# Kernel optimization log

Measured on AMD Instinct MI355X. Metric: run time of the kernel, lower is better.

The kernel has to match this reference:

```python
import jax, jax.numpy as jnp
import numpy as np


def _apply_gates(iou, c_in):
    # iou: [..., 3H]; c_in: [..., H]  (TreeLSTMCell.apply_node_func)
    i, o, u = jnp.split(iou, 3, axis=-1)
    c = jax.nn.sigmoid(i) * jnp.tanh(u) + c_in
    h = jax.nn.sigmoid(o) * jnp.tanh(c)
    return h, c


def setup_inputs() -> dict:
    key = jax.random.key(0)
    ks = jax.random.split(key, 10)
    V, X, H, C = 32000, 300, 256, 5
    B, L = 64, 2048  # 64 perfect binary trees, 2048 leaves each
    s = lambda n: 1.0 / np.sqrt(n)
    return {
        "wordid": jax.random.randint(ks[0], (B, L), 0, V),
        "emb": jax.random.normal(ks[1], (V, X), jnp.float32) * 0.1,
        "W_iou": jax.random.normal(ks[2], (X, 3 * H), jnp.float32) * s(X),
        "b_Wiou": jnp.zeros((3 * H,), jnp.float32),
        "U_iou": jax.random.normal(ks[3], (2 * H, 3 * H), jnp.float32) * s(2 * H),
        "b_Uiou": jnp.zeros((3 * H,), jnp.float32),
        "U_f": jax.random.normal(ks[4], (2 * H, 2 * H), jnp.float32) * s(2 * H),
        "b_Uf": jnp.zeros((2 * H,), jnp.float32),
        "W_out": jax.random.normal(ks[5], (H, C), jnp.float32) * s(H),
        "b_out": jnp.zeros((C,), jnp.float32),
    }


def reference(wordid, emb, W_iou, b_Wiou, U_iou, b_Uiou, U_f, b_Uf, W_out, b_out):
    B, L = wordid.shape
    H = W_out.shape[0]
    # --- leaves: x = W_iou(embed(word)); initial c = 0 ---
    x = emb[wordid]                               # [B, L, X] gather
    iou = x @ W_iou + b_Wiou                      # [B, L, 3H]
    h, c = _apply_gates(iou, jnp.zeros((B, L, H), iou.dtype))
    h_levels = [h.reshape(B * L, H)]
    n = L
    # --- propagate up the tree (topological levels) ---
    while n > 1:
        n //= 2
        h_cat = h.reshape(B, n, 2 * H)            # concat(left,right) per parent
        c_pair = c.reshape(B, n, 2, H)
        f = jax.nn.sigmoid(h_cat @ U_f + b_Uf).reshape(B, n, 2, H)
        c_f = jnp.sum(f * c_pair, axis=2)         # [B, n, H]
        iou = h_cat @ U_iou + b_Uiou              # [B, n, 3H]
        h, c = _apply_gates(iou, c_f)
        h_levels.append(h.reshape(B * n, H))
    h_all = jnp.concatenate(h_levels, axis=0)     # [N_total, H] (level-major)
    # dropout is identity in eval mode
    return h_all @ W_out + b_out                  # [N_total, num_classes]
```

## Files before the change

kernel.cpp:

```cpp
#include <hip/hip_runtime.h>
#include <hip/hip_bf16.h>

typedef __attribute__((ext_vector_type(8))) short bfrag8;
typedef __attribute__((ext_vector_type(4))) float f32x4;

#define DIV_UP(a,b) (((a)+(b)-1)/(b))

__device__ __forceinline__ float sigm(float x){ return 1.0f/(1.0f + __expf(-x)); }
__device__ __forceinline__ float fast_tanh(float x){
  float ax = fabsf(x);
  float t = __expf(-2.0f*ax);
  float r = (1.0f - t)/(1.0f + t);
  return copysignf(r, x);
}
__device__ __forceinline__ float bf2f(short s){
  unsigned int u = ((unsigned int)(unsigned short)s) << 16;
  return __uint_as_float(u);
}
__device__ __forceinline__ unsigned short f2bf_bits(float x){
  __hip_bfloat16 b = __float2bfloat16(x);
  return *reinterpret_cast<unsigned short*>(&b);
}

#define GLOAD_LDS16(g, l) \
  __builtin_amdgcn_global_load_lds((const __attribute__((address_space(1))) void*)(g), \
                                   (__attribute__((address_space(3))) void*)(l), 16, 0, 0)

__global__ void conv_emb4(const float* __restrict__ e, __hip_bfloat16* __restrict__ o){
  int idx = blockIdx.x*256 + threadIdx.x;
  if (idx >= 32000*80) return;
  int v = idx / 80, c = idx - v*80;
  ushort4 r;
  if (c < 75) {
    float4 f = *(const float4*)(e + (size_t)v*300 + c*4);
    r.x = f2bf_bits(f.x); r.y = f2bf_bits(f.y); r.z = f2bf_bits(f.z); r.w = f2bf_bits(f.w);
  } else { r.x = r.y = r.z = r.w = 0; }
  *(ushort4*)((unsigned short*)o + (size_t)v*320 + c*4) = r;
}
__global__ void conv_wiou_i(const float* __restrict__ Wf, __hip_bfloat16* __restrict__ o){
  int idx = blockIdx.x*256 + threadIdx.x;
  if (idx >= 768*320) return;
  int n = idx / 320, k = idx - n*320;
  int eg = n / 48, rem = n - eg*48, gate = rem >> 4, es = rem & 15;
  int e = eg*16 + es;
  o[idx] = __float2bfloat16(k < 300 ? Wf[(size_t)k*768 + gate*256 + e] : 0.0f);
}
__global__ void conv_ucat_i(const float* __restrict__ Ui, const float* __restrict__ Uf,
                            __hip_bfloat16* __restrict__ o){
  int idx = blockIdx.x*256 + threadIdx.x;
  if (idx >= 1280*512) return;
  int n = idx >> 9, k = idx & 511;
  int eg = n / 80, rem = n - eg*80, gate = rem >> 4, es = rem & 15;
  int e = eg*16 + es;
  float v = (gate < 3) ? Ui[(size_t)k*768 + gate*256 + e]
                       : Uf[(size_t)k*512 + (gate-3)*256 + e];
  o[idx] = __float2bfloat16(v);
}

template<int NG, bool G2>
__global__ __launch_bounds__(256, 3) void gemm_fused(
    const char* __restrict__ Ab,
    const int*  __restrict__ wid,
    const char* __restrict__ Btb,
    int M, int K, int Kb,
    const float* __restrict__ b_iou,
    const float* __restrict__ b_f,
    const float* __restrict__ cprev,
    __hip_bfloat16* __restrict__ Hout, float* __restrict__ Cout)
{
  constexpr int GW  = NG*16;
  constexpr int BN  = 2*GW;
  constexpr int BCH = BN*4;
  constexpr int BUF = 8192 + BN*64;
  __shared__ __align__(16) char lds[2*BUF];

  const int lx = blockIdx.y & 7;
  const int ly = ((blockIdx.y >> 3) << 3) | (blockIdx.x & 7);
  const int row0 = ly*128;
  if (row0 >= M) return;

  const int t = threadIdx.x, lane = t & 63, w = t >> 6;
  const int wr = w >> 1, wc = w & 1;
  const int frow = lane & 15, g = lane >> 4;
  const size_t colbase = (size_t)lx * BN;
  const size_t Kbyt = (size_t)K*2;

  const char* abase0[2]; const char* abase1[2];
  #pragma unroll
  for (int i = 0; i < 2; ++i) {
    int c = t + i*256;
    int rp = c >> 3, lc = (c & 7) ^ (rp & 7);
    int r = rp*2 + (lc >> 2), q = lc & 3;
    int row = row0 + r; row = row < M ? row : M-1;
    if constexpr (G2) {
      abase0[i] = Ab + (size_t)wid[2*row]  *512 + q*16;
      abase1[i] = Ab + (size_t)wid[2*row+1]*512 + q*16 - 512;
    } else {
      abase0[i] = Ab + (size_t)row*Kb + q*16;
      abase1[i] = abase0[i];
    }
  }
  const char* bbase[3];
  const int nb = (t < 128) ? ((NG==5) ? 3 : 2) : ((NG==5) ? 2 : 1);
  #pragma unroll
  for (int i = 0; i < 3; ++i) {
    int cb = t + i*256;
    if (cb < BCH) {
      int rp = cb >> 3, lc = (cb & 7) ^ (rp & 7);
      int r = rp*2 + (lc >> 2), q = lc & 3;
      bbase[i] = Btb + (colbase + r)*Kbyt + q*16;
    } else bbase[i] = Btb;
  }

  auto STAGE = [&](int b, int ks){
    const int kb0 = ks*64;
    char* la = lds + b*BUF;
    char* lb = la + 8192;
    #pragma unroll
    for (int i = 0; i < 2; ++i) {
      const char* s = (G2 && kb0 >= 512) ? abase1[i] + kb0 : abase0[i] + kb0;
      GLOAD_LDS16(s, la + (t + i*256)*16);
    }
    #pragma unroll
    for (int i = 0; i < 3; ++i)
      if (i < nb) GLOAD_LDS16(bbase[i] + kb0, lb + (t + i*256)*16);
  };

  const int fr2 = frow >> 1;
  const int pc  = (((frow & 1)*4 + g) ^ (fr2 & 7));
  const int aoff = wr*4096 + fr2*128 + pc*16;
  const int boff = wc*(GW*64) + fr2*128 + pc*16;

  f32x4 acc[4][NG] = {};
  const int nsteps = K >> 5;

  STAGE(0, 0);
  for (int ks = 0; ks < nsteps; ++ks) {
    const int b = ks & 1;
    if (ks + 1 < nsteps) {
      STAGE(b ^ 1, ks + 1);
      if constexpr (NG == 5) {
        if (w < 2) asm volatile("s_waitcnt vmcnt(5)" ::: "memory");
        else       asm volatile("s_waitcnt vmcnt(4)" ::: "memory");
      } else {
        if (w < 2) asm volatile("s_waitcnt vmcnt(4)" ::: "memory");
        else       asm volatile("s_waitcnt vmcnt(3)" ::: "memory");
      }
    } else {
      asm volatile("s_waitcnt vmcnt(0)" ::: "memory");
    }
    __builtin_amdgcn_s_barrier();
    asm volatile("" ::: "memory");

    const char* la = lds + b*BUF;
    const char* lb = la + 8192;
    bfrag8 af[4], bfv[NG];
    #pragma unroll
    for (int mi = 0; mi < 4; ++mi) af[mi] = *(const bfrag8*)(la + aoff + mi*1024);
    #pragma unroll
    for (int gi = 0; gi < NG; ++gi) bfv[gi] = *(const bfrag8*)(lb + boff + gi*1024);
    #pragma unroll
    for (int mi = 0; mi < 4; ++mi)
      #pragma unroll
      for (int gi = 0; gi < NG; ++gi)
        acc[mi][gi] = __builtin_amdgcn_mfma_f32_16x16x32_bf16(af[mi], bfv[gi], acc[mi][gi], 0, 0, 0);

    asm volatile("" ::: "memory");
    __builtin_amdgcn_s_barrier();
  }

  const int e = lx*32 + wc*16 + frow;
  const float bi = b_iou[e], bo = b_iou[256+e], bu = b_iou[512+e];
  float bf0 = 0.f, bf1 = 0.f;
  if constexpr (NG == 5) { bf0 = b_f[e]; bf1 = b_f[256+e]; }
  #pragma unroll
  for (int mi = 0; mi < 4; ++mi) {
    const int mb = row0 + wr*64 + mi*16 + g*4;
    #pragma unroll
    for (int r = 0; r < 4; ++r) {
      const int m = mb + r;
      if (m < M) {
        float cv = sigm(acc[mi][0][r] + bi) * fast_tanh(acc[mi][2][r] + bu);
        if constexpr (NG == 5) {
          const size_t c0i = G2 ? (size_t)wid[2*m]   : (size_t)(2*m);
          const size_t c1i = G2 ? (size_t)wid[2*m+1] : (size_t)(2*m+1);
          cv += sigm(acc[mi][3][r] + bf0) * cprev[c0i*256 + e]
              + sigm(acc[mi][4][r] + bf1) * cprev[c1i*256 + e];
        }
        Cout[(size_t)m*256 + e] = cv;
        Hout[(size_t)m*256 + e] = __float2bfloat16(sigm(acc[mi][1][r] + bo) * fast_tanh(cv));
      }
    }
  }
}

__global__ void outproj_v(const __hip_bfloat16* __restrict__ h, int M,
                          const float* __restrict__ Wout, const float* __restrict__ bout,
                          float* __restrict__ out){
  const int t = threadIdx.x;
  const int half = t >> 5, l32 = t & 31;
  const int e0 = l32 * 8;
  float wv[8][5];
  #pragma unroll
  for (int j = 0; j < 8; ++j)
    #pragma unroll
    for (int cl = 0; cl < 5; ++cl) wv[j][cl] = Wout[(e0+j)*5 + cl];
  const float b0 = bout[0], b1 = bout[1], b2 = bout[2], b3 = bout[3], b4 = bout[4];
  for (int row = blockIdx.x*8 + half; row < M; row += gridDim.x*8) {
    bfrag8 hv = *(const bfrag8*)((const short*)h + (size_t)row*256 + e0);
    float a0=0,a1=0,a2=0,a3=0,a4=0;
    #pragma unroll
    for (int j = 0; j < 8; ++j) {
      float x = bf2f(hv[j]);
      a0 += x*wv[j][0]; a1 += x*wv[j][1]; a2 += x*wv[j][2]; a3 += x*wv[j][3]; a4 += x*wv[j][4];
    }
    #pragma unroll
    for (int off = 16; off; off >>= 1) {
      a0 += __shfl_down(a0, off); a1 += __shfl_down(a1, off);
      a2 += __shfl_down(a2, off); a3 += __shfl_down(a3, off); a4 += __shfl_down(a4, off);
    }
    if (l32 == 0) {
      float* op = out + (size_t)row*5;
      op[0]=a0+b0; op[1]=a1+b1; op[2]=a2+b2; op[3]=a3+b3; op[4]=a4+b4;
    }
  }
}

__global__ void leaf_scatter(const int* __restrict__ wid, const float* __restrict__ outvoc,
                             float* __restrict__ out){
  int p = blockIdx.x*256 + threadIdx.x;
  if (p >= 131072) return;
  const float* s = outvoc + (size_t)wid[p]*5;
  float* d = out + (size_t)p*5;
  #pragma unroll
  for (int j = 0; j < 5; ++j) d[j] = s[j];
}

extern "C" void kernel_launch(void* const* d_in, const int* in_sizes, int n_in,
                              void* d_out, int out_size, void* d_ws, size_t ws_size,
                              hipStream_t stream) {
  const int* wordid   = (const int*)d_in[0];
  const float* emb    = (const float*)d_in[1];
  const float* W_iou  = (const float*)d_in[2];
  const float* b_Wiou = (const float*)d_in[3];
  const float* U_iou  = (const float*)d_in[4];
  const float* b_Uiou = (const float*)d_in[5];
  const float* U_f    = (const float*)d_in[6];
  const float* b_Uf   = (const float*)d_in[7];
  const float* W_out  = (const float*)d_in[8];
  const float* b_out  = (const float*)d_in[9];
  float* out = (float*)d_out;

  char* p = (char*)d_ws;
  auto take = [&](size_t bytes){ char* r = p; p += (bytes + 255) & ~(size_t)255; return r; };
  __hip_bfloat16* wiouT  = (__hip_bfloat16*)take((size_t)768*320*2);
  __hip_bfloat16* ucatT  = (__hip_bfloat16*)take((size_t)1280*512*2);
  __hip_bfloat16* h_voc  = (__hip_bfloat16*)take((size_t)32000*256*2);
  float*          c_voc  = (float*)take((size_t)32000*256*4);
  float*          outvoc = (float*)take((size_t)32000*5*4);
  __hip_bfloat16* hAll   = (__hip_bfloat16*)take((size_t)131008*256*2);
  float*          cA     = (float*)take((size_t)65536*256*4);
  float*          cB     = (float*)take((size_t)32768*256*4);
  __hip_bfloat16* embbf  = (__hip_bfloat16*)cA;

  auto ceil8 = [](int y){ return (y + 7) & ~7; };

  conv_emb4  <<<DIV_UP(32000*80, 256),256,0,stream>>>(emb, embbf);
  conv_wiou_i<<<DIV_UP(768*320,  256),256,0,stream>>>(W_iou, wiouT);
  conv_ucat_i<<<DIV_UP(1280*512, 256),256,0,stream>>>(U_iou, U_f, ucatT);

  gemm_fused<3,false><<<dim3(8,ceil8(250)),256,0,stream>>>(
      (const char*)embbf, nullptr, (const char*)wiouT, 32000, 320, 640,
      b_Wiou, nullptr, nullptr, h_voc, c_voc);
  outproj_v<<<1024,256,0,stream>>>(h_voc, 32000, W_out, b_out, outvoc);
  leaf_scatter<<<DIV_UP(131072,256),256,0,stream>>>(wordid, outvoc, out);

  gemm_fused<5,true><<<dim3(8,512),256,0,stream>>>(
      (const char*)h_voc, wordid, (const char*)ucatT, 65536, 512, 0,
      b_Uiou, b_Uf, c_voc, hAll, cA);

  const __hip_bfloat16* hp = hAll; const float* cp = cA;
  size_t hoff = 65536;
  int Mlvl = 65536;
  for (int lvl = 2; lvl <= 11; ++lvl) {
    Mlvl >>= 1;
    float* cn = (lvl & 1) ? cA : cB;
    gemm_fused<5,false><<<dim3(8,ceil8(DIV_UP(Mlvl,128))),256,0,stream>>>(
        (const char*)hp, nullptr, (const char*)ucatT, Mlvl, 512, 1024,
        b_Uiou, b_Uf, cp, hAll + hoff*256, cn);
    hp = hAll + hoff*256; cp = cn; hoff += Mlvl;
  }

  outproj_v<<<2048,256,0,stream>>>(hAll, 131008, W_out, b_out, out + (size_t)131072*5);
}
```

Baseline: 480.4 us.

## Load A fragments directly to registers and quad-buffer B tiles in LDS

After: 634.1 us. +32.0%, slower.

```diff
diff --git a/kernel.cpp b/kernel.cpp
--- a/kernel.cpp
+++ b/kernel.cpp
@@ -68,11 +68,11 @@
     const float* __restrict__ cprev,
     __hip_bfloat16* __restrict__ Hout, float* __restrict__ Cout)
 {
-  constexpr int GW  = NG*16;
-  constexpr int BN  = 2*GW;
-  constexpr int BCH = BN*4;
-  constexpr int BUF = 8192 + BN*64;
-  __shared__ __align__(16) char lds[2*BUF];
+  constexpr int GW   = NG*16;
+  constexpr int BN   = 2*GW;
+  constexpr int BCH  = BN*4;
+  constexpr int BUFB = BN*64;
+  __shared__ __align__(16) char lds[4*BUFB];
 
   const int lx = blockIdx.y & 7;
   const int ly = ((blockIdx.y >> 3) << 3) | (blockIdx.x & 7);
@@ -85,21 +85,6 @@
   const size_t colbase = (size_t)lx * BN;
   const size_t Kbyt = (size_t)K*2;
 
-  const char* abase0[2]; const char* abase1[2];
-  #pragma unroll
-  for (int i = 0; i < 2; ++i) {
-    int c = t + i*256;
-    int rp = c >> 3, lc = (c & 7) ^ (rp & 7);
-    int r = rp*2 + (lc >> 2), q = lc & 3;
-    int row = row0 + r; row = row < M ? row : M-1;
-    if constexpr (G2) {
-      abase0[i] = Ab + (size_t)wid[2*row]  *512 + q*16;
-      abase1[i] = Ab + (size_t)wid[2*row+1]*512 + q*16 - 512;
-    } else {
-      abase0[i] = Ab + (size_t)row*Kb + q*16;
-      abase1[i] = abase0[i];
-    }
-  }
   const char* bbase[3];
   const int nb = (t < 128) ? ((NG==5) ? 3 : 2) : ((NG==5) ? 2 : 1);
   #pragma unroll
@@ -112,15 +97,31 @@
     } else bbase[i] = Btb;
   }
 
-  auto STAGE = [&](int b, int ks){
-    const int kb0 = ks*64;
-    char* la = lds + b*BUF;
-    char* lb = la + 8192;
-    #pragma unroll
-    for (int i = 0; i < 2; ++i) {
-      const char* s = (G2 && kb0 >= 512) ? abase1[i] + kb0 : abase0[i] + kb0;
-      GLOAD_LDS16(s, la + (t + i*256)*16);
-    }
+  int aoff0[4], aoff1[4];
+  #pragma unroll
+  for (int mi = 0; mi < 4; ++mi) {
+    int row = row0 + wr*64 + mi*16 + frow;
+    row = row < M ? row : M-1;
+    if constexpr (G2) {
+      aoff0[mi] = wid[2*row]*512 + g*16;
+      aoff1[mi] = wid[2*row+1]*512 + g*16 - 512;
+    } else {
+      aoff0[mi] = row*Kb + g*16;
+      aoff1[mi] = aoff0[mi];
+    }
+  }
+
+  bfrag8 af[4];
+  auto ALD = [&](int kb0){
+    #pragma unroll
+    for (int mi = 0; mi < 4; ++mi) {
+      int off = (G2 && kb0 >= 512) ? aoff1[mi] : aoff0[mi];
+      af[mi] = *(const bfrag8*)(Ab + (size_t)(kb0 + off));
+    }
+  };
+  auto BST = [&](int buf, int ks2){
+    const int kb0 = ks2*64;
+    char* lb = lds + buf*BUFB;
     #pragma unroll
     for (int i = 0; i < 3; ++i)
       if (i < nb) GLOAD_LDS16(bbase[i] + kb0, lb + (t + i*256)*16);
@@ -128,35 +129,34 @@
 
   const int fr2 = frow >> 1;
   const int pc  = (((frow & 1)*4 + g) ^ (fr2 & 7));
-  const int aoff = wr*4096 + fr2*128 + pc*16;
   const int boff = wc*(GW*64) + fr2*128 + pc*16;
 
   f32x4 acc[4][NG] = {};
   const int nsteps = K >> 5;
 
-  STAGE(0, 0);
+  BST(0, 0);
+  ALD(0);
+  BST(1, 1);
+
   for (int ks = 0; ks < nsteps; ++ks) {
-    const int b = ks & 1;
     if (ks + 1 < nsteps) {
-      STAGE(b ^ 1, ks + 1);
       if constexpr (NG == 5) {
-        if (w < 2) asm volatile("s_waitcnt vmcnt(5)" ::: "memory");
-        else       asm volatile("s_waitcnt vmcnt(4)" ::: "memory");
+        if (w < 2) asm volatile("s_waitcnt vmcnt(7)" ::: "memory");
+        else       asm volatile("s_waitcnt vmcnt(6)" ::: "memory");
       } else {
-        if (w < 2) asm volatile("s_waitcnt vmcnt(4)" ::: "memory");
-        else       asm volatile("s_waitcnt vmcnt(3)" ::: "memory");
+        if (w < 2) asm volatile("s_waitcnt vmcnt(6)" ::: "memory");
+        else       asm volatile("s_waitcnt vmcnt(5)" ::: "memory");
       }
     } else {
-      asm volatile("s_waitcnt vmcnt(0)" ::: "memory");
+      asm volatile("s_waitcnt vmcnt(4)" ::: "memory");
     }
     __builtin_amdgcn_s_barrier();
     asm volatile("" ::: "memory");
 
-    const char* la = lds + b*BUF;
-    const char* lb = la + 8192;
-    bfrag8 af[4], bfv[NG];
-    #pragma unroll
-    for (int mi = 0; mi < 4; ++mi) af[mi] = *(const bfrag8*)(la + aoff + mi*1024);
+    if (ks + 2 < nsteps) BST((ks + 2) & 3, ks + 2);
+
+    const char* lb = lds + (ks & 3)*BUFB;
+    bfrag8 bfv[NG];
     #pragma unroll
     for (int gi = 0; gi < NG; ++gi) bfv[gi] = *(const bfrag8*)(lb + boff + gi*1024);
     #pragma unroll
@@ -165,8 +165,8 @@
       for (int gi = 0; gi < NG; ++gi)
         acc[mi][gi] = __builtin_amdgcn_mfma_f32_16x16x32_bf16(af[mi], bfv[gi], acc[mi][gi], 0, 0, 0);
 
-    asm volatile("" ::: "memory");
-    __builtin_amdgcn_s_barrier();
+    const int kn = (ks + 1 < nsteps) ? ks + 1 : ks;
+    ALD(kn*64);
   }
 
   const int e = lx*32 + wc*16 + frow;
```
